# Kernel tuning notes

Hardware: AMD Instinct MI355X
Metric: run time of the kernel (lower is better)

## Reference

```python
import jax, jax.numpy as jnp
import numpy as np

N = 50000      # nodes
E = 800000     # edges (avg degree 16)
B = 8          # graphs in batch
H = 128        # hidden (message_passer out_channels)
FF = 64        # fourier_feat_dim -> fourier features have dim 2*FF
REPEATS = 4    # repeats_training
OUT = 4        # output_dim
IN_X = 5
IN_MASK = 3

def _fourier(x, M):
    # https://arxiv.org/pdf/2106.02795.pdf : [cos(xM), sin(xM)] / sqrt(2F)
    p = x @ M
    return jnp.concatenate([jnp.cos(p), jnp.sin(p)], axis=-1) / jnp.sqrt(2.0 * M.shape[1])

def _seg_mean(v, idx, n):
    s = jax.ops.segment_sum(v, idx, num_segments=n)
    c = jax.ops.segment_sum(jnp.ones((v.shape[0],), v.dtype), idx, num_segments=n)
    return s / jnp.maximum(c, 1.0)[:, None]

def setup_inputs() -> dict:
    key = jax.random.key(0)
    ks = jax.random.split(key, 16)
    x = jax.random.normal(ks[0], (N, IN_X), jnp.float32)
    x_mask = jax.random.bernoulli(ks[1], 0.1, (N, IN_MASK)).astype(jnp.float32)
    edge_index = jax.random.randint(ks[2], (2, E), 0, N)
    edge_attr = jax.random.normal(ks[3], (E, 3), jnp.float32)
    pos = jax.random.uniform(ks[4], (N, 2), jnp.float32)
    batch = jnp.sort(jax.random.randint(ks[5], (N,), 0, B))
    sampling_points = jax.random.uniform(ks[6], (2,), jnp.float32)
    fourier_mat = jax.random.normal(ks[7], (2, FF), jnp.float32)  # learnable, init N(0,1)
    W_enc = jax.random.normal(ks[8], (IN_X + IN_MASK, H), jnp.float32) * 0.1
    b_enc = jnp.zeros((H,), jnp.float32)
    W_msg = jax.random.normal(ks[9], (2 * H + 3, H), jnp.float32) * 0.05
    b_msg = jnp.zeros((H,), jnp.float32)
    W_upd = jax.random.normal(ks[10], (4 * H, H), jnp.float32) * 0.05
    b_upd = jnp.zeros((H,), jnp.float32)
    W_dec = jax.random.normal(ks[11], (H, OUT), jnp.float32) * 0.1
    b_dec = jnp.zeros((OUT,), jnp.float32)
    return dict(x=x, x_mask=x_mask, edge_index=edge_index, edge_attr=edge_attr,
                pos=pos, batch=batch, sampling_points=sampling_points,
                fourier_mat=fourier_mat, W_enc=W_enc, b_enc=b_enc,
                W_msg=W_msg, b_msg=b_msg, W_upd=W_upd, b_upd=b_upd,
                W_dec=W_dec, b_dec=b_dec)

def reference(x, x_mask, edge_index, edge_attr, pos, batch, sampling_points,
              fourier_mat, W_enc, b_enc, W_msg, b_msg, W_upd, b_upd, W_dec, b_dec):
    bc = x_mask[:, -1]                                   # 0/1 BC flag
    x_full = jnp.concatenate([x, x_mask], axis=1)        # x = concat([x, x_mask])
    keys_ff = _fourier(pos, fourier_mat)                 # input fourier features [N, 2F]
    h = jax.nn.relu(x_full @ W_enc + b_enc)              # encoder -> [N, H]

    # x_BC: scatter-mean over BC nodes per graph (computed once)
    bc_sum = jax.ops.segment_sum(h * bc[:, None], batch, num_segments=B)
    bc_cnt = jax.ops.segment_sum(bc, batch, num_segments=B)
    x_BC = bc_sum / jnp.maximum(bc_cnt, 1.0)[:, None]    # [B, H]

    x_graph = _seg_mean(h, batch, B)                     # global_mean_pool [B, H]
    src, dst = edge_index[0], edge_index[1]
    deg = jnp.maximum(jax.ops.segment_sum(jnp.ones((E,), h.dtype), dst, num_segments=N), 1.0)

    for _ in range(REPEATS):  # repeated message passing
        m = jax.nn.relu(jnp.concatenate([h[src], h[dst], edge_attr], axis=1) @ W_msg + b_msg)
        agg = jax.ops.segment_sum(m, dst, num_segments=N) / deg[:, None]  # scatter-mean
        upd_in = jnp.concatenate([h, agg, x_graph[batch], x_BC[batch]], axis=1)
        h = h + jax.nn.relu(upd_in @ W_upd + b_upd)
        x_graph = _seg_mean(h, batch, B)                 # re-pool each repeat

    decoded = h @ W_dec + b_dec                          # [N, OUT]

    # kernelized fourier-feature interpolation at the sampling point
    q = _fourier(sampling_points, fourier_mat)           # [2F]
    nq = q / jnp.linalg.norm(q)
    nk = keys_ff / jnp.linalg.norm(keys_ff, axis=1, keepdims=True)
    vals_sum = h.sum(axis=0)                             # [H]
    kwv = nk.T @ h                                       # [2F, H]
    ks_sum = nk.sum(axis=0)                              # [2F]
    enc = (vals_sum + nq @ kwv) / (N + nq @ ks_sum)      # [H]
    U_sampled = enc @ W_dec + b_dec                      # [OUT]
    # pack (U_sampled, decoded) into one array: row 0 = sampled point, rows 1: = nodes
    return jnp.concatenate([U_sampled[None, :], decoded], axis=0)
```

## Files before the change

kernel.cpp:

```cpp
#include <hip/hip_runtime.h>
#include <math.h>

#define Nn 50000
#define Ee 800000
#define Bb 8
#define ROUNDS 4
#define KWVB 512
#define SCB 196
#define AP 40
#define HP 132
#define KS 40
#define NBK 196
#define P1B 391
#define CHUNK 2047

typedef __attribute__((ext_vector_type(8))) short bf16x8;
typedef __attribute__((ext_vector_type(4))) float f32x4;

__device__ inline short f2bf(float f) {
  union { float f; unsigned u; } v; v.f = f;
  unsigned r = v.u + 0x7fff + ((v.u >> 16) & 1);
  return (short)(r >> 16);
}
__device__ inline float bf2f(short s) {
  union { float f; unsigned u; } v; v.u = ((unsigned)(unsigned short)s) << 16;
  return v.f;
}

__global__ __launch_bounds__(256) void encode_seg(
    const float* __restrict__ x, const float* __restrict__ xm,
    const int* __restrict__ batch, const float* __restrict__ W,
    const float* __restrict__ b, float* __restrict__ h,
    float* __restrict__ gsum, float* __restrict__ gcnt,
    float* __restrict__ bcsum, float* __restrict__ bccnt) {
  __shared__ float xs5[128 * 5];
  __shared__ float xm3[128 * 3];
  __shared__ float ls[Bb * 128];
  __shared__ float lb[Bb * 128];
  __shared__ float lc[Bb], lbc[Bb];
  const int t = threadIdx.x;
  const int nBase = blockIdx.x * 128;
  const int j = t & 127, half = t >> 7;
  const int base5 = nBase * 5, base3 = nBase * 3;
  for (int q = t; q < 640; q += 256) xs5[q] = (base5 + q < Nn * 5) ? x[base5 + q] : 0.f;
  for (int q = t; q < 384; q += 256) xm3[q] = (base3 + q < Nn * 3) ? xm[base3 + q] : 0.f;
  for (int q = t; q < Bb * 128; q += 256) { ls[q] = 0.f; lb[q] = 0.f; }
  if (t < Bb) { lc[t] = 0.f; lbc[t] = 0.f; }
  float Wcol[8];
#pragma unroll
  for (int k = 0; k < 8; k++) Wcol[k] = W[k * 128 + j];
  const float bj = b[j];
  __syncthreads();
  int curb = -1;
  float runh = 0.f, runb = 0.f, runc = 0.f, runbc = 0.f;
  for (int kk = 0; kk < 64; kk++) {
    int i = nBase + kk * 2 + half;
    if (i >= Nn) break;
    int li = i - nBase;
    float acc = bj;
#pragma unroll
    for (int k = 0; k < 5; k++) acc = fmaf(xs5[li * 5 + k], Wcol[k], acc);
#pragma unroll
    for (int k = 0; k < 3; k++) acc = fmaf(xm3[li * 3 + k], Wcol[5 + k], acc);
    float v = fmaxf(acc, 0.f);
    h[(size_t)i * 128 + j] = v;
    float bc = xm3[li * 3 + 2];
    int g = batch[i];
    if (g != curb) {
      if (curb >= 0) {
        atomicAdd(&ls[curb * 128 + j], runh);
        atomicAdd(&lb[curb * 128 + j], runb);
        if (j == 0) { atomicAdd(&lc[curb], runc); atomicAdd(&lbc[curb], runbc); }
      }
      curb = g; runh = runb = runc = runbc = 0.f;
    }
    runh += v; runb += v * bc;
    if (j == 0) { runc += 1.f; runbc += bc; }
  }
  if (curb >= 0) {
    atomicAdd(&ls[curb * 128 + j], runh);
    atomicAdd(&lb[curb * 128 + j], runb);
    if (j == 0) { atomicAdd(&lc[curb], runc); atomicAdd(&lbc[curb], runbc); }
  }
  __syncthreads();
  for (int q = t; q < Bb * 128; q += 256) {
    float a = ls[q], c = lb[q];
    if (a != 0.f) atomicAdd(&gsum[q], a);
    if (c != 0.f) atomicAdd(&bcsum[q], c);
  }
  if (t < Bb) { atomicAdd(&gcnt[t], lc[t]); atomicAdd(&bccnt[t], lbc[t]); }
}

__global__ __launch_bounds__(256) void bkt_cnt(
    const int* __restrict__ ei, int* __restrict__ bktcnt,
    const float* __restrict__ Wm, const float* __restrict__ Wu,
    short* __restrict__ Wmt_h, short* __restrict__ Wmt_l,
    short* __restrict__ Wut_h, short* __restrict__ Wut_l) {
  __shared__ int hist[NBK];
  int t = threadIdx.x;
  int idx = blockIdx.x * 256 + t;
  if (idx < 32768) {
    int k = idx & 127, n = (idx >> 7) & 127, y = idx >> 14;
    float w = Wm[(size_t)(y * 128 + k) * 128 + n];
    short hi = f2bf(w);
    Wmt_h[idx] = hi;
    Wmt_l[idx] = f2bf(w - bf2f(hi));
  } else if (idx < 65536) {
    int j = idx - 32768;
    int k = j & 255, n = j >> 8;
    float w = Wu[(size_t)k * 128 + n];
    short hi = f2bf(w);
    Wut_h[j] = hi;
    Wut_l[j] = f2bf(w - bf2f(hi));
  }
  for (int q = t; q < NBK; q += 256) hist[q] = 0;
  __syncthreads();
  int base = blockIdx.x * CHUNK;
  int end = base + CHUNK < Ee ? base + CHUNK : Ee;
  for (int e = base + t; e < end; e += 256) atomicAdd(&hist[ei[Ee + e] >> 8], 1);
  __syncthreads();
  for (int q = t; q < NBK; q += 256)
    if (hist[q]) atomicAdd(&bktcnt[q], hist[q]);
}
__global__ __launch_bounds__(256) void bkt_scan(const int* __restrict__ bktcnt,
                                                int* __restrict__ bktbase,
                                                int* __restrict__ bktcur) {
  __shared__ int s[256];
  int t = threadIdx.x;
  int v = (t < NBK) ? bktcnt[t] : 0;
  s[t] = v;
  __syncthreads();
  for (int off = 1; off < 256; off <<= 1) {
    int x = (t >= off) ? s[t - off] : 0;
    __syncthreads();
    s[t] += x;
    __syncthreads();
  }
  int ex = s[t] - v;
  if (t < NBK) { bktbase[t] = ex; bktcur[t] = ex; }
  if (t == NBK - 1) bktbase[NBK] = ex + v;
}
__global__ __launch_bounds__(256) void bkt_part(
    const int* __restrict__ ei, const float* __restrict__ ea,
    int* __restrict__ bktcur, int2* __restrict__ recA,
    unsigned char* __restrict__ dlo) {
  __shared__ int hist[NBK], lbase[NBK], lcur[NBK];
  int t = threadIdx.x;
  for (int q = t; q < NBK; q += 256) hist[q] = 0;
  __syncthreads();
  int base = blockIdx.x * CHUNK;
  int end = base + CHUNK < Ee ? base + CHUNK : Ee;
  for (int e = base + t; e < end; e += 256) atomicAdd(&hist[ei[Ee + e] >> 8], 1);
  __syncthreads();
  for (int q = t; q < NBK; q += 256) {
    int c = hist[q];
    lbase[q] = c ? atomicAdd(&bktcur[q], c) : 0;
    lcur[q] = 0;
  }
  __syncthreads();
  for (int e = base + t; e < end; e += 256) {
    int d = ei[Ee + e];
    int bk = d >> 8;
    int p = lbase[bk] + atomicAdd(&lcur[bk], 1);
    unsigned r0 = (unsigned)ei[e] |
                  ((unsigned)(unsigned short)f2bf(ea[3 * (size_t)e + 0]) << 16);
    unsigned r1 = (unsigned)(unsigned short)f2bf(ea[3 * (size_t)e + 1]) |
                  ((unsigned)(unsigned short)f2bf(ea[3 * (size_t)e + 2]) << 16);
    recA[p] = make_int2((int)r0, (int)r1);
    dlo[p] = (unsigned char)(d & 255);
  }
}
__global__ __launch_bounds__(256) void dst_cnt_bsum(
    const int* __restrict__ bktbase, const unsigned char* __restrict__ dlo,
    int* __restrict__ cnt, int* __restrict__ bsum) {
  __shared__ int hh[256];
  __shared__ int wsum[4];
  int t = threadIdx.x;
  hh[t] = 0;
  __syncthreads();
  int b = blockIdx.x;
  int lo = bktbase[b], hi = bktbase[b + 1];
  for (int i = lo + t; i < hi; i += 256) atomicAdd(&hh[dlo[i]], 1);
  __syncthreads();
  int d = b * 256 + t;
  int v = hh[t];
  if (d < Nn) cnt[d] = v;
#pragma unroll
  for (int off = 32; off > 0; off >>= 1) v += __shfl_down(v, off);
  if ((t & 63) == 0) wsum[t >> 6] = v;
  __syncthreads();
  if (t == 0) bsum[b] = wsum[0] + wsum[1] + wsum[2] + wsum[3];
}
__global__ __launch_bounds__(256) void scan_top_kernel(const int* __restrict__ bsum,
                                                       int* __restrict__ boff) {
  __shared__ int s[256];
  int t = threadIdx.x;
  int v = (t < SCB) ? bsum[t] : 0;
  s[t] = v;
  __syncthreads();
  for (int off = 1; off < 256; off <<= 1) {
    int x = (t >= off) ? s[t - off] : 0;
    __syncthreads();
    s[t] += x;
    __syncthreads();
  }
  boff[t] = s[t] - v;
}
__global__ __launch_bounds__(256) void apply_fin(
    const int* __restrict__ cnt, const int* __restrict__ boff,
    const int* __restrict__ bktbase, const int2* __restrict__ recA,
    const unsigned char* __restrict__ dlo,
    int* __restrict__ rowptr, float* __restrict__ invdeg,
    int2* __restrict__ rec) {
  __shared__ int s[256];
  __shared__ int cur[256];
  int t = threadIdx.x, b = blockIdx.x;
  int i = b * 256 + t;
  int v = (i < Nn) ? cnt[i] : 0;
  s[t] = v;
  __syncthreads();
  for (int off = 1; off < 256; off <<= 1) {
    int x = (t >= off) ? s[t - off] : 0;
    __syncthreads();
    s[t] += x;
    __syncthreads();
  }
  int ex = boff[b] + s[t] - v;
  if (i < Nn) {
    rowptr[i] = ex;
    invdeg[i] = 1.0f / fmaxf((float)v, 1.0f);
    if (i == Nn - 1) rowptr[Nn] = ex + v;
  }
  cur[t] = ex;
  __syncthreads();
  int lo = bktbase[b], hi = bktbase[b + 1];
  for (int ii = lo + t; ii < hi; ii += 256) {
    int dl = dlo[ii];
    int p = atomicAdd(&cur[dl], 1);
    rec[p] = recA[ii];
  }
}

__global__ __launch_bounds__(256) void proj_mfma(
    const float* __restrict__ h, const short* __restrict__ Wth,
    unsigned char* __restrict__ hs8, unsigned short* __restrict__ hdbf,
    const float* __restrict__ bcsum, const float* __restrict__ bccnt,
    const float* __restrict__ bu, const float* __restrict__ Wu,
    float* __restrict__ gbst, const float* __restrict__ gsum_in,
    const float* __restrict__ gcnt, float* __restrict__ gb_out, int dogbst) {
  __shared__ short Ah_s[64 * AP];
  __shared__ short Bh_s[256 * AP];
  const int t = threadIdx.x;
  const int nBase = blockIdx.x * 64;
  const int wave = t >> 6, lane = t & 63;
  const int ml = lane & 15, quad = lane >> 4;
  const int ko = quad * 8;

  if (blockIdx.x < Bb) {
    float* xgs = (float*)Bh_s;
    const int g = blockIdx.x;
    if (dogbst) {
      if (t < 128) xgs[t] = bcsum[g * 128 + t] / fmaxf(bccnt[g], 1.f);
      __syncthreads();
      if (t < 128) {
        float a = bu[t];
#pragma unroll 4
        for (int k = 0; k < 128; k++) a = fmaf(xgs[k], Wu[(size_t)(384 + k) * 128 + t], a);
        gbst[g * 128 + t] = a;
      }
      __syncthreads();
    }
    if (t < 128) xgs[t] = gsum_in[g * 128 + t] / fmaxf(gcnt[g], 1.f);
    __syncthreads();
    if (t < 128) {
      float a = gbst[g * 128 + t];
#pragma unroll 4
      for (int k = 0; k < 128; k++) a = fmaf(xgs[k], Wu[(size_t)(256 + k) * 128 + t], a);
      gb_out[g * 128 + t] = a;
    }
  }

  f32x4 acc[4][4];
#pragma unroll
  for (int yn = 0; yn < 4; yn++)
#pragma unroll
    for (int mt = 0; mt < 4; mt++)
#pragma unroll
      for (int q = 0; q < 4; q++) acc[yn][mt][q] = 0.f;

  const int arow = t >> 2;
  const int kq = (t & 3) * 8;
  const int nd0 = nBase + arow;
  const int nn = nd0 < Nn ? nd0 : Nn - 1;

  for (int c = 0; c < 4; c++) {
    const int k0 = c * 32;
    const float* p = &h[(size_t)nn * 128 + k0 + kq];
    float4 u0 = *(const float4*)(p + 0);
    float4 u1 = *(const float4*)(p + 4);
    const bf16x8 w0 = *(const bf16x8*)&Wth[(size_t)t * 128 + k0];
    const bf16x8 w1 = *(const bf16x8*)&Wth[(size_t)t * 128 + k0 + 8];
    const bf16x8 w2 = *(const bf16x8*)&Wth[(size_t)t * 128 + k0 + 16];
    const bf16x8 w3 = *(const bf16x8*)&Wth[(size_t)t * 128 + k0 + 24];
    float xs[8] = {u0.x, u0.y, u0.z, u0.w, u1.x, u1.y, u1.z, u1.w};
    bf16x8 vh0;
#pragma unroll
    for (int j = 0; j < 8; j++) vh0[j] = f2bf(xs[j]);
    __syncthreads();
    *(bf16x8*)&Ah_s[arow * AP + kq] = vh0;
    *(bf16x8*)&Bh_s[t * AP + 0] = w0;
    *(bf16x8*)&Bh_s[t * AP + 8] = w1;
    *(bf16x8*)&Bh_s[t * AP + 16] = w2;
    *(bf16x8*)&Bh_s[t * AP + 24] = w3;
    __syncthreads();
#pragma unroll
    for (int mt = 0; mt < 4; mt++) {
      const int ar = (mt * 16 + ml) * AP + ko;
      bf16x8 ah = *(const bf16x8*)&Ah_s[ar];
#pragma unroll
      for (int y = 0; y < 2; y++) {
#pragma unroll
        for (int nt = 0; nt < 2; nt++) {
          const int br = (y * 128 + wave * 32 + nt * 16 + ml) * AP + ko;
          bf16x8 bh = *(const bf16x8*)&Bh_s[br];
          acc[y * 2 + nt][mt] = __builtin_amdgcn_mfma_f32_16x16x32_bf16(ah, bh, acc[y * 2 + nt][mt], 0, 0, 0);
        }
      }
    }
  }
#pragma unroll
  for (int nt = 0; nt < 2; nt++) {
    const int ch = wave * 32 + nt * 16 + ml;
#pragma unroll
    for (int mt = 0; mt < 4; mt++) {
#pragma unroll
      for (int q = 0; q < 4; q++) {
        int nd = nBase + mt * 16 + quad * 4 + q;
        if (nd < Nn) {
          int pk = __builtin_amdgcn_cvt_pk_fp8_f32(acc[nt][mt][q], acc[nt][mt][q], 0, false);
          hs8[(size_t)nd * 128 + ch] = (unsigned char)(pk & 0xff);
          hdbf[(size_t)nd * 128 + ch] = (unsigned short)f2bf(acc[2 + nt][mt][q]);
        }
      }
    }
  }
}

__global__ __launch_bounds__(256) void agg_kernel(
    const unsigned char* __restrict__ hs8, const unsigned short* __restrict__ hdbf,
    unsigned short* __restrict__ aggbf, const int2* __restrict__ rec,
    const int* __restrict__ rowptr, const float* __restrict__ invdeg,
    const float* __restrict__ Wm, const float* __restrict__ bm) {
  int t = threadIdx.x;
  int hw = t >> 5, lane = t & 31;
  int v = blockIdx.x * 8 + hw;
  if (v >= Nn) return;
  int c0 = lane * 4;
  const float4 We0 = *(const float4*)&Wm[(size_t)256 * 128 + c0];
  const float4 We1 = *(const float4*)&Wm[(size_t)257 * 128 + c0];
  const float4 We2 = *(const float4*)&Wm[(size_t)258 * 128 + c0];
  const float4 b4  = *(const float4*)&bm[c0];
  const ushort4 hd4 = *(const ushort4*)&hdbf[(size_t)v * 128 + c0];
  const float bx = b4.x + bf2f((short)hd4.x), by = b4.y + bf2f((short)hd4.y),
              bz = b4.z + bf2f((short)hd4.z), bw = b4.w + bf2f((short)hd4.w);
  float ax = 0.f, ay = 0.f, az = 0.f, aw = 0.f;
  float ax2 = 0.f, ay2 = 0.f, az2 = 0.f, aw2 = 0.f;
  const int r0 = rowptr[v], r1 = rowptr[v + 1];
  int e = r0;
  for (; e + 2 <= r1; e += 2) {
    int2 q0 = rec[e], q1 = rec[e + 1];
    int s0 = q0.x & 0xffff, s1 = q1.x & 0xffff;
    unsigned hr0 = *(const unsigned*)&hs8[(size_t)s0 * 128 + c0];
    unsigned hr1 = *(const unsigned*)&hs8[(size_t)s1 * 128 + c0];
    float e00 = bf2f((short)(q0.x >> 16));
    float e01 = bf2f((short)(q0.y & 0xffff));
    float e02 = bf2f((short)(q0.y >> 16));
    float e10 = bf2f((short)(q1.x >> 16));
    float e11 = bf2f((short)(q1.y & 0xffff));
    float e12 = bf2f((short)(q1.y >> 16));
    float h0x = __builtin_amdgcn_cvt_f32_fp8(hr0, 0);
    float h0y = __builtin_amdgcn_cvt_f32_fp8(hr0, 1);
    float h0z = __builtin_amdgcn_cvt_f32_fp8(hr0, 2);
    float h0w = __builtin_amdgcn_cvt_f32_fp8(hr0, 3);
    float h1x = __builtin_amdgcn_cvt_f32_fp8(hr1, 0);
    float h1y = __builtin_amdgcn_cvt_f32_fp8(hr1, 1);
    float h1z = __builtin_amdgcn_cvt_f32_fp8(hr1, 2);
    float h1w = __builtin_amdgcn_cvt_f32_fp8(hr1, 3);
    ax += fmaxf(fmaf(e00, We0.x, fmaf(e01, We1.x, fmaf(e02, We2.x, h0x + bx))), 0.f);
    ay += fmaxf(fmaf(e00, We0.y, fmaf(e01, We1.y, fmaf(e02, We2.y, h0y + by))), 0.f);
    az += fmaxf(fmaf(e00, We0.z, fmaf(e01, We1.z, fmaf(e02, We2.z, h0z + bz))), 0.f);
    aw += fmaxf(fmaf(e00, We0.w, fmaf(e01, We1.w, fmaf(e02, We2.w, h0w + bw))), 0.f);
    ax2 += fmaxf(fmaf(e10, We0.x, fmaf(e11, We1.x, fmaf(e12, We2.x, h1x + bx))), 0.f);
    ay2 += fmaxf(fmaf(e10, We0.y, fmaf(e11, We1.y, fmaf(e12, We2.y, h1y + by))), 0.f);
    az2 += fmaxf(fmaf(e10, We0.z, fmaf(e11, We1.z, fmaf(e12, We2.z, h1z + bz))), 0.f);
    aw2 += fmaxf(fmaf(e10, We0.w, fmaf(e11, We1.w, fmaf(e12, We2.w, h1w + bw))), 0.f);
  }
  if (e < r1) {
    int2 q0 = rec[e];
    int s0 = q0.x & 0xffff;
    unsigned hr0 = *(const unsigned*)&hs8[(size_t)s0 * 128 + c0];
    float e00 = bf2f((short)(q0.x >> 16));
    float e01 = bf2f((short)(q0.y & 0xffff));
    float e02 = bf2f((short)(q0.y >> 16));
    float h0x = __builtin_amdgcn_cvt_f32_fp8(hr0, 0);
    float h0y = __builtin_amdgcn_cvt_f32_fp8(hr0, 1);
    float h0z = __builtin_amdgcn_cvt_f32_fp8(hr0, 2);
    float h0w = __builtin_amdgcn_cvt_f32_fp8(hr0, 3);
    ax += fmaxf(fmaf(e00, We0.x, fmaf(e01, We1.x, fmaf(e02, We2.x, h0x + bx))), 0.f);
    ay += fmaxf(fmaf(e00, We0.y, fmaf(e01, We1.y, fmaf(e02, We2.y, h0y + by))), 0.f);
    az += fmaxf(fmaf(e00, We0.z, fmaf(e01, We1.z, fmaf(e02, We2.z, h0z + bz))), 0.f);
    aw += fmaxf(fmaf(e00, We0.w, fmaf(e01, We1.w, fmaf(e02, We2.w, h0w + bw))), 0.f);
  }
  const float idg = invdeg[v];
  ushort4 o;
  o.x = (unsigned short)f2bf((ax + ax2) * idg);
  o.y = (unsigned short)f2bf((ay + ay2) * idg);
  o.z = (unsigned short)f2bf((az + az2) * idg);
  o.w = (unsigned short)f2bf((aw + aw2) * idg);
  *(ushort4*)&aggbf[(size_t)v * 128 + c0] = o;
}

__global__ __launch_bounds__(256) void updg_mfma(
    float* __restrict__ h, const unsigned short* __restrict__ aggbf,
    const int* __restrict__ batch,
    const short* __restrict__ Wth, const short* __restrict__ Wtl,
    const float* __restrict__ gb, float* __restrict__ gsum_out) {
  __shared__ short Ah_s[64 * AP], Al_s[64 * AP];
  __shared__ short Bh_s[128 * AP], Bl_s[128 * AP];
  __shared__ float gbs[Bb * 128];
  __shared__ float ls[Bb * 128];
  const int t = threadIdx.x;
  const int nBase = blockIdx.x * 64;
  *(float4*)&gbs[t * 4] = *(const float4*)&gb[t * 4];
#pragma unroll
  for (int q = 0; q < 4; q++) ls[t + q * 256] = 0.f;

  const int wave = t >> 6, lane = t & 63;
  const int ml = lane & 15, quad = lane >> 4;
  const int ko = quad * 8;

  f32x4 acc[2][4];
#pragma unroll
  for (int nt = 0; nt < 2; nt++)
#pragma unroll
    for (int mt = 0; mt < 4; mt++)
#pragma unroll
      for (int q = 0; q < 4; q++) acc[nt][mt][q] = 0.f;

  const int arow = t >> 2;
  const int kq = (t & 3) * 8;
  const int brow = t >> 1;
  const int kc = (t & 1) * 16;
  const int nd0 = nBase + arow;
  const int nn = nd0 < Nn ? nd0 : Nn - 1;

  for (int c = 0; c < 8; c++) {
    const int k0 = c * 32;
    bf16x8 vh0, vl0;
    if (c < 4) {
      const float* p = &h[(size_t)nn * 128 + k0 + kq];
      float4 u0 = *(const float4*)(p + 0);
      float4 u1 = *(const float4*)(p + 4);
      float xs[8] = {u0.x, u0.y, u0.z, u0.w, u1.x, u1.y, u1.z, u1.w};
#pragma unroll
      for (int j = 0; j < 8; j++) {
        short hi = f2bf(xs[j]);
        vh0[j] = hi; vl0[j] = f2bf(xs[j] - bf2f(hi));
      }
    } else {
      vh0 = *(const bf16x8*)&aggbf[(size_t)nn * 128 + (c - 4) * 32 + kq];
    }
    const bf16x8 gb0 = *(const bf16x8*)&Wth[(size_t)brow * 256 + k0 + kc];
    const bf16x8 gb1 = *(const bf16x8*)&Wth[(size_t)brow * 256 + k0 + kc + 8];
    const bf16x8 gl0 = *(const bf16x8*)&Wtl[(size_t)brow * 256 + k0 + kc];
    const bf16x8 gl1 = *(const bf16x8*)&Wtl[(size_t)brow * 256 + k0 + kc + 8];
    __syncthreads();
    *(bf16x8*)&Ah_s[arow * AP + kq] = vh0;
    if (c < 4) *(bf16x8*)&Al_s[arow * AP + kq] = vl0;
    *(bf16x8*)&Bh_s[brow * AP + kc] = gb0;
    *(bf16x8*)&Bh_s[brow * AP + kc + 8] = gb1;
    *(bf16x8*)&Bl_s[brow * AP + kc] = gl0;
    *(bf16x8*)&Bl_s[brow * AP + kc + 8] = gl1;
    __syncthreads();
    if (c < 4) {
#pragma unroll
      for (int mt = 0; mt < 4; mt++) {
        const int ar = (mt * 16 + ml) * AP + ko;
        bf16x8 ah = *(const bf16x8*)&Ah_s[ar];
        bf16x8 al = *(const bf16x8*)&Al_s[ar];
#pragma unroll
        for (int nt = 0; nt < 2; nt++) {
          const int br = (wave * 32 + nt * 16 + ml) * AP + ko;
          bf16x8 bh = *(const bf16x8*)&Bh_s[br];
          bf16x8 bl = *(const bf16x8*)&Bl_s[br];
          acc[nt][mt] = __builtin_amdgcn_mfma_f32_16x16x32_bf16(ah, bh, acc[nt][mt], 0, 0, 0);
          acc[nt][mt] = __builtin_amdgcn_mfma_f32_16x16x32_bf16(ah, bl, acc[nt][mt], 0, 0, 0);
          acc[nt][mt] = __builtin_amdgcn_mfma_f32_16x16x32_bf16(al, bh, acc[nt][mt], 0, 0, 0);
        }
      }
    } else {
#pragma unroll
      for (int mt = 0; mt < 4; mt++) {
        const int ar = (mt * 16 + ml) * AP + ko;
        bf16x8 ah = *(const bf16x8*)&Ah_s[ar];
#pragma unroll
        for (int nt = 0; nt < 2; nt++) {
          const int br = (wave * 32 + nt * 16 + ml) * AP + ko;
          bf16x8 bh = *(const bf16x8*)&Bh_s[br];
          bf16x8 bl = *(const bf16x8*)&Bl_s[br];
          acc[nt][mt] = __builtin_amdgcn_mfma_f32_16x16x32_bf16(ah, bh, acc[nt][mt], 0, 0, 0);
          acc[nt][mt] = __builtin_amdgcn_mfma_f32_16x16x32_bf16(ah, bl, acc[nt][mt], 0, 0, 0);
        }
      }
    }
  }
#pragma unroll
  for (int nt = 0; nt < 2; nt++) {
    const int ch = wave * 32 + nt * 16 + ml;
#pragma unroll
    for (int mt = 0; mt < 4; mt++) {
      int rbase = nBase + mt * 16 + quad * 4;
      float runv = 0.f;
      int curb = -1;
#pragma unroll
      for (int q = 0; q < 4; q++) {
        int nd = rbase + q;
        if (nd < Nn) {
          int bi = batch[nd];
          float u = fmaxf(acc[nt][mt][q] + gbs[bi * 128 + ch], 0.f);
          float hn = h[(size_t)nd * 128 + ch] + u;
          h[(size_t)nd * 128 + ch] = hn;
          if (bi != curb) {
            if (curb >= 0) atomicAdd(&ls[curb * 128 + ch], runv);
            curb = bi;
            runv = 0.f;
          }
          runv += hn;
        }
      }
      if (curb >= 0) atomicAdd(&ls[curb * 128 + ch], runv);
    }
  }
  __syncthreads();
#pragma unroll
  for (int q = 0; q < 4; q++) {
    int idx = t + q * 256;
    float v = ls[idx];
    if (v != 0.f) atomicAdd(&gsum_out[idx], v);
  }
}

__global__ __launch_bounds__(256) void kwv_kernel(
    const float* __restrict__ h, const float* __restrict__ pos,
    const float* __restrict__ Fm, const float* __restrict__ Wd,
    const float* __restrict__ bd, float* __restrict__ partial,
    float* __restrict__ ksum, float* __restrict__ out) {
  __shared__ float h_s[32 * HP];
  __shared__ short nkT[128 * KS];
  __shared__ short hT[128 * KS];
  __shared__ float wd[512];
  __shared__ float ksum_s[128];
  __shared__ float dsum[256];
  const int t = threadIdx.x;
  const int hr = t >> 3;
  const int hc = (t & 7) * 16;
  const int fg = (t & 7) * 8;
  const int wave = t >> 6, lane = t & 63;
  const int ml = lane & 15, quad = lane >> 4;
  const int ko = quad * 8;
  if (t < 128) { *(float4*)&wd[t * 4] = *(const float4*)&Wd[t * 4]; ksum_s[t] = 0.f; }
  const float bdv = bd[t & 3];
  const int dn = (t & 127) >> 2, dno = t & 3;
  const int dk0 = (t >> 7) * 64;
  f32x4 acc[2][8];
#pragma unroll
  for (int nt = 0; nt < 2; nt++)
#pragma unroll
    for (int mt = 0; mt < 8; mt++)
#pragma unroll
      for (int q = 0; q < 4; q++) acc[nt][mt][q] = 0.f;
  float klc[8], kls[8];
#pragma unroll
  for (int f = 0; f < 8; f++) { klc[f] = 0.f; kls[f] = 0.f; }

  int ptile = -1;
  const int nTiles = (Nn + 31) / 32;
  for (int tile = blockIdx.x; tile < nTiles; tile += gridDim.x) {
    const int gh = tile * 32 + hr;
    float4 hv0 = {0.f, 0.f, 0.f, 0.f}, hv1 = hv0, hv2 = hv0, hv3 = hv0;
    float cbuf[8], sbuf[8];
    if (gh < Nn) {
      const float* hp = &h[(size_t)gh * 128 + hc];
      hv0 = *(const float4*)(hp + 0);
      hv1 = *(const float4*)(hp + 4);
      hv2 = *(const float4*)(hp + 8);
      hv3 = *(const float4*)(hp + 12);
      const float px = pos[gh * 2 + 0], py = pos[gh * 2 + 1];
#pragma unroll
      for (int f = 0; f < 8; f++) {
        float p = px * Fm[fg + f] + py * Fm[64 + fg + f];
        cbuf[f] = cosf(p) * 0.125f;
        sbuf[f] = sinf(p) * 0.125f;
      }
    } else {
#pragma unroll
      for (int f = 0; f < 8; f++) { cbuf[f] = 0.f; sbuf[f] = 0.f; }
    }
    float xs[16] = {hv0.x,hv0.y,hv0.z,hv0.w, hv1.x,hv1.y,hv1.z,hv1.w,
                    hv2.x,hv2.y,hv2.z,hv2.w, hv3.x,hv3.y,hv3.z,hv3.w};
    __syncthreads();
    if (ptile >= 0 && t < 128) {
      int gn = ptile * 32 + dn;
      if (gn < Nn) out[4 + (size_t)gn * 4 + dno] = dsum[t] + dsum[t + 128] + bdv;
    }
    *(float4*)&h_s[hr * HP + hc + 0]  = hv0;
    *(float4*)&h_s[hr * HP + hc + 4]  = hv1;
    *(float4*)&h_s[hr * HP + hc + 8]  = hv2;
    *(float4*)&h_s[hr * HP + hc + 12] = hv3;
#pragma unroll
    for (int i = 0; i < 16; i++) hT[(hc + i) * KS + hr] = f2bf(xs[i]);
#pragma unroll
    for (int f = 0; f < 8; f++) {
      nkT[(fg + f) * KS + hr] = f2bf(cbuf[f]);
      nkT[(64 + fg + f) * KS + hr] = f2bf(sbuf[f]);
      klc[f] += cbuf[f];
      kls[f] += sbuf[f];
    }
    __syncthreads();
#pragma unroll
    for (int mt = 0; mt < 8; mt++) {
      bf16x8 ah = *(const bf16x8*)&nkT[(mt * 16 + ml) * KS + ko];
#pragma unroll
      for (int nt = 0; nt < 2; nt++) {
        bf16x8 bh = *(const bf16x8*)&hT[(wave * 32 + nt * 16 + ml) * KS + ko];
        acc[nt][mt] = __builtin_amdgcn_mfma_f32_16x16x32_bf16(ah, bh, acc[nt][mt], 0, 0, 0);
      }
    }
    {
      float s = 0.f;
#pragma unroll 4
      for (int kk = dk0; kk < dk0 + 64; kk++) {
        int k = (kk + dn) & 127;
        s = fmaf(h_s[dn * HP + k], wd[k * 4 + dno], s);
      }
      dsum[t] = s;
    }
    ptile = tile;
  }
  __syncthreads();
  if (ptile >= 0 && t < 128) {
    int gn = ptile * 32 + dn;
    if (gn < Nn) out[4 + (size_t)gn * 4 + dno] = dsum[t] + dsum[t + 128] + bdv;
  }
  float* pb = &partial[(size_t)blockIdx.x * 16384];
#pragma unroll
  for (int nt = 0; nt < 2; nt++) {
    const int col = wave * 32 + nt * 16 + ml;
#pragma unroll
    for (int mt = 0; mt < 8; mt++) {
#pragma unroll
      for (int q = 0; q < 4; q++) {
        int row = mt * 16 + quad * 4 + q;
        pb[row * 128 + col] = acc[nt][mt][q];
      }
    }
  }
#pragma unroll
  for (int f = 0; f < 8; f++) {
    atomicAdd(&ksum_s[fg + f], klc[f]);
    atomicAdd(&ksum_s[64 + fg + f], kls[f]);
  }
  __syncthreads();
  if (t < 128) atomicAdd(&ksum[t], ksum_s[t]);
}

__global__ __launch_bounds__(256) void kwv_reduce(const float* __restrict__ partial,
                                                  float* __restrict__ kwv) {
  int idx = blockIdx.x * 256 + threadIdx.x;
  float s = 0.f;
  for (int b = 0; b < KWVB; b++) s += partial[(size_t)b * 16384 + idx];
  kwv[idx] = s;
}

__global__ __launch_bounds__(128) void final_kernel(
    const float* __restrict__ sp, const float* __restrict__ Fm,
    const float* __restrict__ kwv, const float* __restrict__ vs,
    const float* __restrict__ ksum, const float* __restrict__ Wd,
    const float* __restrict__ bd, float* __restrict__ out) {
  __shared__ float nq_s[128];
  __shared__ float red[2];
  __shared__ float redU[8];
  int t = threadIdx.x;
  int jj = t & 63;
  float p = sp[0] * Fm[jj] + sp[1] * Fm[64 + jj];
  nq_s[t] = ((t < 64) ? cosf(p) : sinf(p)) * 0.125f;
  __syncthreads();
  float num = 0.f;
#pragma unroll
  for (int g = 0; g < Bb; g++) num += vs[g * 128 + t];
  for (int k = 0; k < 128; k++) num = fmaf(nq_s[k], kwv[k * 128 + t], num);
  float dp = nq_s[t] * ksum[t];
#pragma unroll
  for (int off = 32; off > 0; off >>= 1) dp += __shfl_down(dp, off);
  if ((t & 63) == 0) red[t >> 6] = dp;
  __syncthreads();
  float den = (float)Nn + red[0] + red[1];
  float e = num / den;
  float u[4];
#pragma unroll
  for (int o = 0; o < 4; o++) u[o] = e * Wd[t * 4 + o];
#pragma unroll
  for (int off = 32; off > 0; off >>= 1) {
#pragma unroll
    for (int o = 0; o < 4; o++) u[o] += __shfl_down(u[o], off);
  }
  if ((t & 63) == 0) {
#pragma unroll
    for (int o = 0; o < 4; o++) redU[(t >> 6) * 4 + o] = u[o];
  }
  __syncthreads();
  if (t < 4) out[t] = redU[t] + redU[4 + t] + bd[t];
}

extern "C" void kernel_launch(void* const* d_in, const int* in_sizes, int n_in,
                              void* d_out, int out_size, void* d_ws, size_t ws_size,
                              hipStream_t stream) {
  const float* x    = (const float*)d_in[0];
  const float* xm   = (const float*)d_in[1];
  const int*   ei   = (const int*)d_in[2];
  const float* ea   = (const float*)d_in[3];
  const float* pos  = (const float*)d_in[4];
  const int*   batch= (const int*)d_in[5];
  const float* sp   = (const float*)d_in[6];
  const float* Fm   = (const float*)d_in[7];
  const float* Wenc = (const float*)d_in[8];
  const float* benc = (const float*)d_in[9];
  const float* Wmsg = (const float*)d_in[10];
  const float* bmsg = (const float*)d_in[11];
  const float* Wupd = (const float*)d_in[12];
  const float* bupd = (const float*)d_in[13];
  const float* Wdec = (const float*)d_in[14];
  const float* bdec = (const float*)d_in[15];
  float* out = (float*)d_out;

  float* ws     = (float*)d_ws;
  float* h      = ws;
  float* agg    = h + (size_t)Nn * 128;
  float* aux    = agg + (size_t)Nn * 128;
  float* invdeg = aux + (size_t)Nn * 128;
  float* gsum   = invdeg + Nn;
  float* gcnt   = gsum + 1024;
  float* bcsum  = gcnt + 8;
  float* bccnt  = bcsum + 1024;
  float* gsumR  = bccnt + 8;
  float* vsum   = gsumR + 4096;
  float* ksum   = vsum + 128;
  int*   bktcnt = (int*)(ksum + 128);
  float* gbst   = (float*)(bktcnt + 196);
  float* gbuf   = gbst + 1024;
  float* kwv    = gbuf + 4096;
  int2*  rec    = (int2*)(kwv + 16384);
  int*   cnt    = (int*)(rec + Ee);
  int*   rowptr = cnt + Nn;
  int*   bsum   = rowptr + Nn + 1;
  int*   boff   = bsum + 256;
  int*   bktbase= boff + 256;
  int*   bktcur = bktbase + 197;
  short* wmt_h  = (short*)(bktcur + 196);
  short* wmt_l  = wmt_h + 32768;
  short* wut_h  = wmt_l + 32768;
  short* wut_l  = wut_h + 32768;
  int2*  recA   = (int2*)(wut_l + 32768);
  unsigned char* dlo = (unsigned char*)(recA + Ee);

  unsigned short* aggbf = (unsigned short*)agg;
  unsigned char*  hs8   = (unsigned char*)aux;
  unsigned short* hdbf  = (unsigned short*)(hs8 + (size_t)Nn * 128);

  hipMemsetAsync(gsum, 0, 6612 * 4, stream);

  bkt_cnt<<<P1B, 256, 0, stream>>>(ei, bktcnt, Wmsg, Wupd,
                                   wmt_h, wmt_l, wut_h, wut_l);
  bkt_scan<<<1, 256, 0, stream>>>(bktcnt, bktbase, bktcur);
  bkt_part<<<P1B, 256, 0, stream>>>(ei, ea, bktcur, recA, dlo);
  dst_cnt_bsum<<<NBK, 256, 0, stream>>>(bktbase, dlo, cnt, bsum);
  scan_top_kernel<<<1, 256, 0, stream>>>(bsum, boff);
  apply_fin<<<NBK, 256, 0, stream>>>(cnt, boff, bktbase, recA, dlo,
                                     rowptr, invdeg, rec);

  const int nb128 = (Nn + 127) / 128;
  const int nb64  = (Nn + 63) / 64;
  encode_seg<<<nb128, 256, 0, stream>>>(x, xm, batch, Wenc, benc, h,
                                        gsum, gcnt, bcsum, bccnt);

  for (int r = 0; r < ROUNDS; r++) {
    proj_mfma<<<nb64, 256, 0, stream>>>(
        h, wmt_h, hs8, hdbf,
        bcsum, bccnt, bupd, Wupd, gbst,
        (r == 0) ? gsum : (gsumR + (size_t)(r - 1) * 1024), gcnt,
        gbuf + (size_t)r * 1024, (r == 0) ? 1 : 0);
    agg_kernel<<<(Nn + 7) / 8, 256, 0, stream>>>(hs8, hdbf, aggbf, rec, rowptr,
                                                 invdeg, Wmsg, bmsg);
    updg_mfma<<<nb64, 256, 0, stream>>>(h, aggbf, batch, wut_h, wut_l,
                                        gbuf + (size_t)r * 1024,
                                        gsumR + (size_t)r * 1024);
  }

  kwv_kernel<<<KWVB, 256, 0, stream>>>(h, pos, Fm, Wdec, bdec, agg, ksum, out);
  kwv_reduce<<<64, 256, 0, stream>>>(agg, kwv);
  final_kernel<<<1, 128, 0, stream>>>(sp, Fm, kwv, gsumR + 3 * 1024, ksum,
                                      Wdec, bdec, out);
}
```

Measured before the change: 623.7 us.

## Fuse next-round message projection into update kernel and graph bias into aggregation

The per-round projection of h through the message weights is moved into the tail of the update kernel. The freshly updated h tile is staged as bf16 in shared memory and multiplied with MFMA there, so h is not re-read from global memory and one launch per round disappears. The per-graph bias computation is moved into the first blocks of the aggregation kernel, and only the first round runs the standalone projection. The cost is more shared memory and registers in the update kernel, which may lower occupancy. The projection input also changes from fp32 h to bf16-rounded h.

```diff
diff --git a/kernel.cpp b/kernel.cpp
--- a/kernel.cpp
+++ b/kernel.cpp
@@ -10,6 +10,7 @@
 #define AP 40
 #define HP 132
 #define KS 40
+#define HTT 136
 #define NBK 196
 #define P1B 391
 #define CHUNK 2047
@@ -247,7 +248,7 @@
     const float* __restrict__ bcsum, const float* __restrict__ bccnt,
     const float* __restrict__ bu, const float* __restrict__ Wu,
     float* __restrict__ gbst, const float* __restrict__ gsum_in,
-    const float* __restrict__ gcnt, float* __restrict__ gb_out, int dogbst) {
+    const float* __restrict__ gcnt, float* __restrict__ gb_out) {
   __shared__ short Ah_s[64 * AP];
   __shared__ short Bh_s[256 * AP];
   const int t = threadIdx.x;
@@ -259,17 +260,15 @@
   if (blockIdx.x < Bb) {
     float* xgs = (float*)Bh_s;
     const int g = blockIdx.x;
-    if (dogbst) {
-      if (t < 128) xgs[t] = bcsum[g * 128 + t] / fmaxf(bccnt[g], 1.f);
-      __syncthreads();
-      if (t < 128) {
-        float a = bu[t];
+    if (t < 128) xgs[t] = bcsum[g * 128 + t] / fmaxf(bccnt[g], 1.f);
+    __syncthreads();
+    if (t < 128) {
+      float a = bu[t];
 #pragma unroll 4
-        for (int k = 0; k < 128; k++) a = fmaf(xgs[k], Wu[(size_t)(384 + k) * 128 + t], a);
-        gbst[g * 128 + t] = a;
-      }
-      __syncthreads();
-    }
+      for (int k = 0; k < 128; k++) a = fmaf(xgs[k], Wu[(size_t)(384 + k) * 128 + t], a);
+      gbst[g * 128 + t] = a;
+    }
+    __syncthreads();
     if (t < 128) xgs[t] = gsum_in[g * 128 + t] / fmaxf(gcnt[g], 1.f);
     __syncthreads();
     if (t < 128) {
@@ -350,8 +349,23 @@
     const unsigned char* __restrict__ hs8, const unsigned short* __restrict__ hdbf,
     unsigned short* __restrict__ aggbf, const int2* __restrict__ rec,
     const int* __restrict__ rowptr, const float* __restrict__ invdeg,
-    const float* __restrict__ Wm, const float* __restrict__ bm) {
+    const float* __restrict__ Wm, const float* __restrict__ bm,
+    const float* __restrict__ Wu, const float* __restrict__ gbst,
+    const float* __restrict__ gsum_in, const float* __restrict__ gcnt,
+    float* __restrict__ gb_out, int dogb) {
+  __shared__ float xgs[128];
   int t = threadIdx.x;
+  if (dogb && blockIdx.x < Bb) {
+    const int g = blockIdx.x;
+    if (t < 128) xgs[t] = gsum_in[g * 128 + t] / fmaxf(gcnt[g], 1.f);
+    __syncthreads();
+    if (t < 128) {
+      float a = gbst[g * 128 + t];
+#pragma unroll 4
+      for (int k = 0; k < 128; k++) a = fmaf(xgs[k], Wu[(size_t)(256 + k) * 128 + t], a);
+      gb_out[g * 128 + t] = a;
+    }
+  }
   int hw = t >> 5, lane = t & 31;
   int v = blockIdx.x * 8 + hw;
   if (v >= Nn) return;
@@ -420,15 +434,22 @@
   *(ushort4*)&aggbf[(size_t)v * 128 + c0] = o;
 }
 
-__global__ __launch_bounds__(256) void updg_mfma(
+__global__ __launch_bounds__(256) void updg_proj(
     float* __restrict__ h, const unsigned short* __restrict__ aggbf,
     const int* __restrict__ batch,
     const short* __restrict__ Wth, const short* __restrict__ Wtl,
-    const float* __restrict__ gb, float* __restrict__ gsum_out) {
-  __shared__ short Ah_s[64 * AP], Al_s[64 * AP];
-  __shared__ short Bh_s[128 * AP], Bl_s[128 * AP];
+    const float* __restrict__ gb, float* __restrict__ gsum_out,
+    const short* __restrict__ Wmth, unsigned char* __restrict__ hs8,
+    unsigned short* __restrict__ hdbf, int doproj) {
+  __shared__ short ms[15360];
   __shared__ float gbs[Bb * 128];
   __shared__ float ls[Bb * 128];
+  short* Ah_s = ms;
+  short* Al_s = ms + 64 * AP;
+  short* Bh_s = ms + 2 * 64 * AP;
+  short* Bl_s = ms + 2 * 64 * AP + 128 * AP;
+  short* hnT  = ms;
+
   const int t = threadIdx.x;
   const int nBase = blockIdx.x * 64;
   *(float4*)&gbs[t * 4] = *(const float4*)&gb[t * 4];
@@ -514,22 +535,27 @@
       }
     }
   }
+  __syncthreads();
+
 #pragma unroll
   for (int nt = 0; nt < 2; nt++) {
     const int ch = wave * 32 + nt * 16 + ml;
 #pragma unroll
     for (int mt = 0; mt < 4; mt++) {
-      int rbase = nBase + mt * 16 + quad * 4;
+      int lrb = mt * 16 + quad * 4;
+      int rbase = nBase + lrb;
       float runv = 0.f;
       int curb = -1;
 #pragma unroll
       for (int q = 0; q < 4; q++) {
         int nd = rbase + q;
+        short hv = 0;
         if (nd < Nn) {
           int bi = batch[nd];
           float u = fmaxf(acc[nt][mt][q] + gbs[bi * 128 + ch], 0.f);
           float hn = h[(size_t)nd * 128 + ch] + u;
           h[(size_t)nd * 128 + ch] = hn;
+          hv = f2bf(hn);
           if (bi != curb) {
             if (curb >= 0) atomicAdd(&ls[curb * 128 + ch], runv);
             curb = bi;
@@ -537,6 +563,7 @@
           }
           runv += hn;
         }
+        hnT[(lrb + q) * HTT + ch] = hv;
       }
       if (curb >= 0) atomicAdd(&ls[curb * 128 + ch], runv);
     }
@@ -547,6 +574,60 @@
     int idx = t + q * 256;
     float v = ls[idx];
     if (v != 0.f) atomicAdd(&gsum_out[idx], v);
+  }
+
+  if (doproj) {
+#pragma unroll 1
+    for (int y = 0; y < 2; y++) {
+      f32x4 pacc[2][4];
+#pragma unroll
+      for (int nt = 0; nt < 2; nt++)
+#pragma unroll
+        for (int mt = 0; mt < 4; mt++)
+#pragma unroll
+          for (int q = 0; q < 4; q++) pacc[nt][mt][q] = 0.f;
+#pragma unroll
+      for (int c = 0; c < 4; c++) {
+        const bf16x8 b0 = *(const bf16x8*)&Wmth[(size_t)(y * 128 + wave * 32 + ml) * 128 + c * 32 + ko];
+        const bf16x8 b1 = *(const bf16x8*)&Wmth[(size_t)(y * 128 + wave * 32 + 16 + ml) * 128 + c * 32 + ko];
+#pragma unroll
+        for (int mt = 0; mt < 4; mt++) {
+          bf16x8 ah = *(const bf16x8*)&hnT[(mt * 16 + ml) * HTT + c * 32 + ko];
+          pacc[0][mt] = __builtin_amdgcn_mfma_f32_16x16x32_bf16(ah, b0, pacc[0][mt], 0, 0, 0);
+          pacc[1][mt] = __builtin_amdgcn_mfma_f32_16x16x32_bf16(ah, b1, pacc[1][mt], 0, 0, 0);
+        }
+      }
+      if (y == 0) {
+#pragma unroll
+        for (int nt = 0; nt < 2; nt++) {
+          const int ch = wave * 32 + nt * 16 + ml;
+#pragma unroll
+          for (int mt = 0; mt < 4; mt++) {
+#pragma unroll
+            for (int q = 0; q < 4; q++) {
+              int nd = nBase + mt * 16 + quad * 4 + q;
+              if (nd < Nn) {
+                int pk = __builtin_amdgcn_cvt_pk_fp8_f32(pacc[nt][mt][q], pacc[nt][mt][q], 0, false);
+                hs8[(size_t)nd * 128 + ch] = (unsigned char)(pk & 0xff);
+              }
+            }
+          }
+        }
+      } else {
+#pragma unroll
+        for (int nt = 0; nt < 2; nt++) {
+          const int ch = wave * 32 + nt * 16 + ml;
+#pragma unroll
+          for (int mt = 0; mt < 4; mt++) {
+#pragma unroll
+            for (int q = 0; q < 4; q++) {
+              int nd = nBase + mt * 16 + quad * 4 + q;
+              if (nd < Nn) hdbf[(size_t)nd * 128 + ch] = (unsigned short)f2bf(pacc[nt][mt][q]);
+            }
+          }
+        }
+      }
+    }
   }
 }
 
@@ -793,17 +874,20 @@
   encode_seg<<<nb128, 256, 0, stream>>>(x, xm, batch, Wenc, benc, h,
                                         gsum, gcnt, bcsum, bccnt);
 
+  proj_mfma<<<nb64, 256, 0, stream>>>(h, wmt_h, hs8, hdbf,
+                                      bcsum, bccnt, bupd, Wupd, gbst,
+                                      gsum, gcnt, gbuf);
+
   for (int r = 0; r < ROUNDS; r++) {
-    proj_mfma<<<nb64, 256, 0, stream>>>(
-        h, wmt_h, hs8, hdbf,
-        bcsum, bccnt, bupd, Wupd, gbst,
+    agg_kernel<<<(Nn + 7) / 8, 256, 0, stream>>>(
+        hs8, hdbf, aggbf, rec, rowptr, invdeg, Wmsg, bmsg,
+        Wupd, gbst,
         (r == 0) ? gsum : (gsumR + (size_t)(r - 1) * 1024), gcnt,
-        gbuf + (size_t)r * 1024, (r == 0) ? 1 : 0);
-    agg_kernel<<<(Nn + 7) / 8, 256, 0, stream>>>(hs8, hdbf, aggbf, rec, rowptr,
-                                                 invdeg, Wmsg, bmsg);
-    updg_mfma<<<nb64, 256, 0, stream>>>(h, aggbf, batch, wut_h, wut_l,
-                                        gbuf + (size_t)r * 1024,
-                                        gsumR + (size_t)r * 1024);
+        gbuf + (size_t)r * 1024, (r >= 1) ? 1 : 0);
+    updg_proj<<<nb64, 256, 0, stream>>>(
+        h, aggbf, batch, wut_h, wut_l,
+        gbuf + (size_t)r * 1024, gsumR + (size_t)r * 1024,
+        wmt_h, hs8, hdbf, (r < ROUNDS - 1) ? 1 : 0);
   }
 
   kwv_kernel<<<KWVB, 256, 0, stream>>>(h, pos, Fm, Wdec, bdec, agg, ksum, out);
```

Result: no change. 617.8 us (-0.9%).
